# Performance work log

Hardware: AMD Instinct MI355X
Metric: run time of the kernel (lower is better)

The kernel has to match this reference:

```python
import jax, jax.numpy as jnp
import numpy as np

N_NODES = 50000
N_EDGES = 200000
D_FEAT = 512
D_HID = 1024


def setup_inputs() -> dict:
    key = jax.random.key(0)
    k_x, k_s, k_d, k_w1, k_w2 = jax.random.split(key, 5)
    x = jax.random.normal(k_x, (N_NODES, D_FEAT), dtype=jnp.float32)
    src = jax.random.randint(k_s, (N_EDGES,), 0, N_NODES, dtype=jnp.int64)
    dst = jax.random.randint(k_d, (N_EDGES,), 0, N_NODES, dtype=jnp.int64)
    # MLP params: Linear(2d -> hidden), ReLU, Linear(hidden -> 1)
    W1 = jax.random.normal(k_w1, (2 * D_FEAT, D_HID), dtype=jnp.float32) * (1.0 / np.sqrt(2 * D_FEAT))
    b1 = jnp.zeros((D_HID,), dtype=jnp.float32)
    W2 = jax.random.normal(k_w2, (D_HID, 1), dtype=jnp.float32) * (1.0 / np.sqrt(D_HID))
    b2 = jnp.zeros((1,), dtype=jnp.float32)
    return {"x": x, "src": src, "dst": dst, "W1": W1, "b1": b1, "W2": W2, "b2": b2}


def reference(x, src, dst, W1, b1, W2, b2):
    # Per-edge gather of src/dst node embeddings, concat along feature dim
    h = jnp.concatenate([x[src], x[dst]], axis=1)          # [E, 2d]
    h = jax.nn.relu(h @ W1 + b1)                            # [E, hidden]
    score = h @ W2 + b2                                     # [E, 1]
    return score
```

## Files before the change

### kernel.cpp

```cpp
#include <hip/hip_runtime.h>
#include <cstdint>
#include <cstddef>

typedef __attribute__((ext_vector_type(8))) short short8;
typedef __attribute__((ext_vector_type(4))) float f32x4;

#define D_FEAT 512
#define D_HID  1024
#define NCOL   2048
#define NCHUNK 32

__device__ __forceinline__ unsigned short f2bf(float f) {
    unsigned u = __builtin_bit_cast(unsigned, f);
    u += 0x7FFFu + ((u >> 16) & 1u);
    return (unsigned short)(u >> 16);
}

#define FENCE() asm volatile("" ::: "memory")
#define BAR()   do { FENCE(); __builtin_amdgcn_s_barrier(); FENCE(); } while (0)

__global__ __launch_bounds__(256) void cast_x_kernel(const float* __restrict__ x,
                                                     unsigned short* __restrict__ xb,
                                                     int n) {
    int i = (blockIdx.x * 256 + threadIdx.x) * 8;
    if (i >= n) return;
    const float4* xp = (const float4*)(x + i);
    float4 a = xp[0], b = xp[1];
    short8 o;
    o[0] = (short)f2bf(a.x); o[1] = (short)f2bf(a.y);
    o[2] = (short)f2bf(a.z); o[3] = (short)f2bf(a.w);
    o[4] = (short)f2bf(b.x); o[5] = (short)f2bf(b.y);
    o[6] = (short)f2bf(b.z); o[7] = (short)f2bf(b.w);
    *(short8*)(xb + i) = o;
}

__global__ __launch_bounds__(256) void transpose_w1_kernel(const float* __restrict__ W1,
                                                           unsigned short* __restrict__ w1t) {
    __shared__ float tile[32][33];
    const int half = blockIdx.z;
    const int kb = blockIdx.y * 32;
    const int nb = blockIdx.x * 32;
    const int tx = threadIdx.x, ty = threadIdx.y;
    #pragma unroll
    for (int i = 0; i < 32; i += 8)
        tile[ty + i][tx] = W1[(size_t)(half * 512 + kb + ty + i) * 1024 + nb + tx];
    __syncthreads();
    #pragma unroll
    for (int i = 0; i < 32; i += 8)
        w1t[(size_t)(half * 1024 + nb + ty + i) * 512 + kb + tx] = f2bf(tile[tx][ty + i]);
}

#define BM 256
#define BN 256
#define BK 64
#define GM 32
#define NB2 (NCOL / BN)

__global__ __launch_bounds__(512, 2) void gemm_uv_kernel(
    const unsigned short* __restrict__ xb,
    const unsigned short* __restrict__ w1t,
    const float* __restrict__ b1,
    unsigned char* __restrict__ qUV,
    float* __restrict__ scales,
    int M, int MB)
{
    __shared__ __align__(16) unsigned short smem[65536];

    const int bid = blockIdx.x;
    int g    = bid / (GM * NB2);
    int rem  = bid - g * (GM * NB2);
    int base = g * GM;
    int gm   = MB - base; if (gm > GM) gm = GM;
    int mb   = base + rem % gm;
    int nb   = rem / gm;
    const int m0 = mb * BM;
    const int n0 = nb * BN;

    const int tid  = threadIdx.x;
    const int wave = tid >> 6;
    const int lane = tid & 63;
    const int q    = lane >> 4;
    const int l15  = lane & 15;
    const int wr   = wave >> 2;
    const int wc   = wave & 3;

    const int ar    = lane >> 3;
    const int swcol = ((lane & 7) ^ ar) * 8;
    const int swz   = l15 & 7;

    const int slotA0 = wr * 16 + wc * 4;
    int bslot[4];
    bslot[0] = wc * 8 + wr * 2;     bslot[1] = bslot[0] + 1;
    bslot[2] = wc * 8 + 4 + wr * 2; bslot[3] = bslot[2] + 1;

    int rowA[4], rowB[4];
    #pragma unroll
    for (int j = 0; j < 4; ++j) {
        int m = m0 + (slotA0 + j) * 8 + ar;
        rowA[j] = (m < M) ? m : (M - 1);
        rowB[j] = n0 + bslot[j] * 8 + ar;
    }

    unsigned short* const sAbuf[2] = { smem,         smem + 16384 };
    unsigned short* const sBbuf[2] = { smem + 32768, smem + 49152 };

    auto stageA2 = [&](int t, int cb, int j0) {
        const int k0 = t * BK;
        #pragma unroll
        for (int j = 0; j < 2; ++j)
            __builtin_amdgcn_global_load_lds(
                (const __attribute__((address_space(1))) void*)(xb + ((size_t)rowA[j0 + j] << 9) + k0 + swcol),
                (__attribute__((address_space(3))) void*)(sAbuf[cb] + (slotA0 + j0 + j) * 512),
                16, 0, 0);
    };
    auto stageB2 = [&](int t, int cb, int j0) {
        const int k0 = t * BK;
        #pragma unroll
        for (int j = 0; j < 2; ++j)
            __builtin_amdgcn_global_load_lds(
                (const __attribute__((address_space(1))) void*)(w1t + ((size_t)rowB[j0 + j] << 9) + k0 + swcol),
                (__attribute__((address_space(3))) void*)(sBbuf[cb] + bslot[j0 + j] * 512),
                16, 0, 0);
    };
    auto readA = [&](int cb, int mt, int ks) -> short8 {
        int row = wr * 128 + mt * 16 + l15;
        return *(const short8*)(sAbuf[cb] + row * 64 + (((q | (ks << 2)) ^ swz) * 8));
    };
    auto readB = [&](int cb, int nt, int ks) -> short8 {
        int row = wc * 64 + nt * 16 + l15;
        return *(const short8*)(sBbuf[cb] + row * 64 + (((q | (ks << 2)) ^ swz) * 8));
    };

    float b1v[4];
    #pragma unroll
    for (int nt = 0; nt < 4; ++nt) {
        int n = n0 + wc * 64 + nt * 16 + l15;
        b1v[nt] = (n < D_HID) ? b1[n] : 0.f;
    }
    f32x4 acc[8][4];
    #pragma unroll
    for (int i = 0; i < 8; ++i)
        #pragma unroll
        for (int j = 0; j < 4; ++j)
            acc[i][j] = (f32x4){b1v[j], b1v[j], b1v[j], b1v[j]};

    stageA2(0, 0, 0);
    stageA2(0, 0, 2);
    stageB2(0, 0, 0);
    stageB2(0, 0, 2);
    stageA2(1, 1, 0);
    asm volatile("s_waitcnt vmcnt(4)" ::: "memory");
    BAR();

    short8 aR[4][2], bA[2][2], bB[2][2];

    #pragma unroll
    for (int t = 0; t < 8; ++t) {
        const int c = t & 1;

        #pragma unroll
        for (int mt = 0; mt < 4; ++mt)
            #pragma unroll
            for (int ks = 0; ks < 2; ++ks)
                aR[mt][ks] = readA(c, mt, ks);
        #pragma unroll
        for (int nt = 0; nt < 2; ++nt)
            #pragma unroll
            for (int ks = 0; ks < 2; ++ks)
                bA[nt][ks] = readB(c, nt, ks);
        if (t < 7) stageA2(t + 1, c ^ 1, 2);
        BAR();
        __builtin_amdgcn_s_setprio(1);
        #pragma unroll
        for (int ks = 0; ks < 2; ++ks)
            #pragma unroll
            for (int mt = 0; mt < 4; ++mt)
                #pragma unroll
                for (int nt = 0; nt < 2; ++nt)
                    acc[mt][nt] = __builtin_amdgcn_mfma_f32_16x16x32_bf16(aR[mt][ks], bA[nt][ks], acc[mt][nt], 0, 0, 0);
        __builtin_amdgcn_s_setprio(0);
        if (t < 7) { asm volatile("s_waitcnt vmcnt(4)" ::: "memory"); }
        else       { asm volatile("s_waitcnt vmcnt(0)" ::: "memory"); }
        BAR();

        #pragma unroll
        for (int nt = 0; nt < 2; ++nt)
            #pragma unroll
            for (int ks = 0; ks < 2; ++ks)
                bB[nt][ks] = readB(c, 2 + nt, ks);
        if (t < 7) stageB2(t + 1, c ^ 1, 0);
        BAR();
        __builtin_amdgcn_s_setprio(1);
        #pragma unroll
        for (int ks = 0; ks < 2; ++ks)
            #pragma unroll
            for (int mt = 0; mt < 4; ++mt)
                #pragma unroll
                for (int nt = 0; nt < 2; ++nt)
                    acc[mt][2 + nt] = __builtin_amdgcn_mfma_f32_16x16x32_bf16(aR[mt][ks], bB[nt][ks], acc[mt][2 + nt], 0, 0, 0);
        __builtin_amdgcn_s_setprio(0);
        BAR();

        #pragma unroll
        for (int mt = 0; mt < 4; ++mt)
            #pragma unroll
            for (int ks = 0; ks < 2; ++ks)
                aR[mt][ks] = readA(c, 4 + mt, ks);
        if (t < 7) stageB2(t + 1, c ^ 1, 2);
        BAR();
        __builtin_amdgcn_s_setprio(1);
        #pragma unroll
        for (int ks = 0; ks < 2; ++ks)
            #pragma unroll
            for (int mt = 0; mt < 4; ++mt)
                #pragma unroll
                for (int nt = 0; nt < 2; ++nt)
                    acc[4 + mt][nt] = __builtin_amdgcn_mfma_f32_16x16x32_bf16(aR[mt][ks], bA[nt][ks], acc[4 + mt][nt], 0, 0, 0);
        __builtin_amdgcn_s_setprio(0);
        BAR();

        if (t < 6) stageA2(t + 2, c, 0);
        BAR();
        __builtin_amdgcn_s_setprio(1);
        #pragma unroll
        for (int ks = 0; ks < 2; ++ks)
            #pragma unroll
            for (int mt = 0; mt < 4; ++mt)
                #pragma unroll
                for (int nt = 0; nt < 2; ++nt)
                    acc[4 + mt][2 + nt] = __builtin_amdgcn_mfma_f32_16x16x32_bf16(aR[mt][ks], bB[nt][ks], acc[4 + mt][2 + nt], 0, 0, 0);
        __builtin_amdgcn_s_setprio(0);
        if (t < 6)      { asm volatile("s_waitcnt vmcnt(4)" ::: "memory"); }
        else if (t == 6){ asm volatile("s_waitcnt vmcnt(2)" ::: "memory"); }
        BAR();
    }

    float msc[8], minv[8];
    #pragma unroll
    for (int mt = 0; mt < 8; ++mt) {
        float m_ = 1e-30f;
        #pragma unroll
        for (int nt = 0; nt < 4; ++nt)
            #pragma unroll
            for (int r = 0; r < 4; ++r)
                m_ = fmaxf(m_, fabsf(acc[mt][nt][r]));
        #pragma unroll
        for (int off = 1; off < 64; off <<= 1)
            m_ = fmaxf(m_, __shfl_xor(m_, off));
        msc[mt]  = m_ * (1.0f / 127.0f);
        minv[mt] = 127.0f * __builtin_amdgcn_rcpf(m_);
    }

    unsigned char* ep8 = (unsigned char*)smem + wave * 8192;
    const float MAGIC = 12583040.0f;
    #pragma unroll
    for (int mt = 0; mt < 8; ++mt)
        #pragma unroll
        for (int nt = 0; nt < 4; ++nt)
            #pragma unroll
            for (int r = 0; r < 4; ++r) {
                float f = fmaf(acc[mt][nt][r], minv[mt], MAGIC);
                ep8[(mt * 16 + q * 4 + r) * 64 + ((nt ^ q) * 16) + l15] =
                    (unsigned char)__builtin_bit_cast(unsigned, f);
            }
    const int chunk = (n0 + wc * 64) >> 6;
    #pragma unroll
    for (int h = 0; h < 2; ++h) {
        int srow = m0 + wr * 128 + h * 64 + q * 16 + l15;
        if (srow < M) scales[(size_t)srow * NCHUNK + chunk] = msc[h * 4 + q];
    }
    #pragma unroll
    for (int it = 0; it < 8; ++it) {
        int flat = it * 64 + lane;
        int r   = flat >> 2;
        int cI  = flat & 3;
        int m   = m0 + wr * 128 + r;
        if (m < M) {
            int4 v = *(const int4*)(ep8 + r * 64 + ((cI ^ ((r >> 2) & 3)) * 16));
            *(int4*)(qUV + (size_t)m * NCOL + n0 + wc * 64 + cI * 16) = v;
        }
    }
}

__global__ __launch_bounds__(256) void edge_score_kernel(
    const unsigned char* __restrict__ qUV,
    const float* __restrict__ scales,
    const int* __restrict__ src, const int* __restrict__ dst,
    const float* __restrict__ W2, const float* __restrict__ b2,
    float* __restrict__ out, int E)
{
    const int wave = threadIdx.x >> 6;
    const int lane = threadIdx.x & 63;
    const int gw = blockIdx.x * 4 + wave;
    const int e0 = gw * 2;
    const int e1 = e0 + 1;
    if (e0 >= E) return;
    const bool has1 = (e1 < E);

    const int s0 = src[e0];
    const int d0 = dst[e0];
    const int s1 = has1 ? src[e1] : s0;
    const int d1 = has1 ? dst[e1] : d0;

    uint4 qu0 = *(const uint4*)(qUV + (size_t)s0 * NCOL + lane * 16);
    uint4 qv0 = *(const uint4*)(qUV + (size_t)d0 * NCOL + D_HID + lane * 16);
    uint4 qu1 = *(const uint4*)(qUV + (size_t)s1 * NCOL + lane * 16);
    uint4 qv1 = *(const uint4*)(qUV + (size_t)d1 * NCOL + D_HID + lane * 16);
    const int ch = lane >> 2;
    float su0 = scales[(size_t)s0 * NCHUNK + ch];
    float sv0 = scales[(size_t)d0 * NCHUNK + 16 + ch];
    float su1 = scales[(size_t)s1 * NCHUNK + ch];
    float sv1 = scales[(size_t)d1 * NCHUNK + 16 + ch];
    float cc0 = -128.0f * (su0 + sv0);
    float cc1 = -128.0f * (su1 + sv1);

    const float4* wp = (const float4*)(W2 + lane * 16);
    float4 wa = wp[0], wb = wp[1], wc = wp[2], wd = wp[3];
    float w[16] = {wa.x, wa.y, wa.z, wa.w, wb.x, wb.y, wb.z, wb.w,
                   wc.x, wc.y, wc.z, wc.w, wd.x, wd.y, wd.z, wd.w};
    const float bias = b2[0];

    const unsigned* u0w = (const unsigned*)&qu0; const unsigned* v0w = (const unsigned*)&qv0;
    const unsigned* u1w = (const unsigned*)&qu1; const unsigned* v1w = (const unsigned*)&qv1;

    float acc0 = 0.f, acc1 = 0.f;
    #pragma unroll
    for (int dw = 0; dw < 4; ++dw) {
        #pragma unroll
        for (int b = 0; b < 4; ++b) {
            int k = dw * 4 + b;
            float ub0 = (float)((u0w[dw] >> (8 * b)) & 0xFFu);
            float vb0 = (float)((v0w[dw] >> (8 * b)) & 0xFFu);
            float h0 = fmaf(ub0, su0, fmaf(vb0, sv0, cc0));
            acc0 = fmaf(fmaxf(h0, 0.f), w[k], acc0);
            float ub1 = (float)((u1w[dw] >> (8 * b)) & 0xFFu);
            float vb1 = (float)((v1w[dw] >> (8 * b)) & 0xFFu);
            float h1 = fmaf(ub1, su1, fmaf(vb1, sv1, cc1));
            acc1 = fmaf(fmaxf(h1, 0.f), w[k], acc1);
        }
    }
    #pragma unroll
    for (int off = 1; off < 64; off <<= 1) {
        acc0 += __shfl_xor(acc0, off);
        acc1 += __shfl_xor(acc1, off);
    }
    if (lane == 0) out[e0] = acc0 + bias;
    if (lane == 1 && has1) out[e1] = acc1 + bias;
}

extern "C" void kernel_launch(void* const* d_in, const int* in_sizes, int n_in,
                              void* d_out, int out_size, void* d_ws, size_t ws_size,
                              hipStream_t stream) {
    const float* x   = (const float*)d_in[0];
    const int*   src = (const int*)d_in[1];
    const int*   dst = (const int*)d_in[2];
    const float* W1  = (const float*)d_in[3];
    const float* b1  = (const float*)d_in[4];
    const float* W2  = (const float*)d_in[5];
    const float* b2  = (const float*)d_in[6];
    float* out = (float*)d_out;

    const int M = in_sizes[0] / D_FEAT;
    const int E = in_sizes[1];

    char* ws = (char*)d_ws;
    unsigned char*  qUV    = (unsigned char*)ws;
    float*          scales = (float*)(ws + (size_t)M * NCOL);
    unsigned short* xb     = (unsigned short*)(ws + (size_t)M * NCOL + (size_t)M * NCHUNK * 4);
    unsigned short* w1t    = (unsigned short*)(ws + (size_t)M * NCOL + (size_t)M * NCHUNK * 4
                                                  + (size_t)M * D_FEAT * 2);

    const int nx = M * D_FEAT;
    cast_x_kernel<<<(nx / 8 + 255) / 256, 256, 0, stream>>>(x, xb, nx);
    transpose_w1_kernel<<<dim3(32, 16, 2), dim3(32, 8), 0, stream>>>(W1, w1t);
    const int MB = (M + BM - 1) / BM;
    gemm_uv_kernel<<<MB * NB2, 512, 0, stream>>>(xb, w1t, b1, qUV, scales, M, MB);
    edge_score_kernel<<<(E + 7) / 8, 256, 0, stream>>>(qUV, scales, src, dst, W2, b2, out, E);
}
```

Baseline: 363.1 us.

## Make GEMM persistent with epilogue/prefetch overlap and merge prep kernels

Merges the x cast and W1 transpose into a single prep launch. The GEMM becomes a persistent kernel with 256 blocks, each looping over M-tiles with a stride of 32. It issues the next tile's first stage loads before running the quantization epilogue of the current tile, and uses separate LDS regions for the epilogue so the two can overlap. This is meant to cut launch overhead and hide the epilogue and tail latency. In exchange it drops the grouped M-tile swizzle and the deeper two-ahead A prefetch inside the k-loop, which could hurt L2 reuse or load pipelining.

After: 477.5 us. 1.32x slower.

```diff
diff --git a/kernel.cpp b/kernel.cpp
--- a/kernel.cpp
+++ b/kernel.cpp
@@ -19,41 +19,44 @@
 #define FENCE() asm volatile("" ::: "memory")
 #define BAR()   do { FENCE(); __builtin_amdgcn_s_barrier(); FENCE(); } while (0)
 
-__global__ __launch_bounds__(256) void cast_x_kernel(const float* __restrict__ x,
-                                                     unsigned short* __restrict__ xb,
-                                                     int n) {
-    int i = (blockIdx.x * 256 + threadIdx.x) * 8;
-    if (i >= n) return;
-    const float4* xp = (const float4*)(x + i);
-    float4 a = xp[0], b = xp[1];
-    short8 o;
-    o[0] = (short)f2bf(a.x); o[1] = (short)f2bf(a.y);
-    o[2] = (short)f2bf(a.z); o[3] = (short)f2bf(a.w);
-    o[4] = (short)f2bf(b.x); o[5] = (short)f2bf(b.y);
-    o[6] = (short)f2bf(b.z); o[7] = (short)f2bf(b.w);
-    *(short8*)(xb + i) = o;
-}
-
-__global__ __launch_bounds__(256) void transpose_w1_kernel(const float* __restrict__ W1,
-                                                           unsigned short* __restrict__ w1t) {
-    __shared__ float tile[32][33];
-    const int half = blockIdx.z;
-    const int kb = blockIdx.y * 32;
-    const int nb = blockIdx.x * 32;
-    const int tx = threadIdx.x, ty = threadIdx.y;
-    #pragma unroll
-    for (int i = 0; i < 32; i += 8)
-        tile[ty + i][tx] = W1[(size_t)(half * 512 + kb + ty + i) * 1024 + nb + tx];
-    __syncthreads();
-    #pragma unroll
-    for (int i = 0; i < 32; i += 8)
-        w1t[(size_t)(half * 1024 + nb + ty + i) * 512 + kb + tx] = f2bf(tile[tx][ty + i]);
+#define NCAST 12500
+
+__global__ __launch_bounds__(256) void prep_kernel(const float* __restrict__ x,
+                                                   unsigned short* __restrict__ xb,
+                                                   const float* __restrict__ W1,
+                                                   unsigned short* __restrict__ w1t,
+                                                   int n) {
+    if ((int)blockIdx.x < NCAST) {
+        int i = (blockIdx.x * 256 + threadIdx.x) * 8;
+        if (i >= n) return;
+        const float4* xp = (const float4*)(x + i);
+        float4 a = xp[0], b = xp[1];
+        short8 o;
+        o[0] = (short)f2bf(a.x); o[1] = (short)f2bf(a.y);
+        o[2] = (short)f2bf(a.z); o[3] = (short)f2bf(a.w);
+        o[4] = (short)f2bf(b.x); o[5] = (short)f2bf(b.y);
+        o[6] = (short)f2bf(b.z); o[7] = (short)f2bf(b.w);
+        *(short8*)(xb + i) = o;
+    } else {
+        __shared__ float tile[32][33];
+        const int bid2 = blockIdx.x - NCAST;
+        const int half = bid2 >> 9;
+        const int kb   = ((bid2 >> 5) & 15) * 32;
+        const int nb   = (bid2 & 31) * 32;
+        const int tx = threadIdx.x & 31, ty = threadIdx.x >> 5;
+        #pragma unroll
+        for (int i = 0; i < 32; i += 8)
+            tile[ty + i][tx] = W1[(size_t)(half * 512 + kb + ty + i) * 1024 + nb + tx];
+        __syncthreads();
+        #pragma unroll
+        for (int i = 0; i < 32; i += 8)
+            w1t[(size_t)(half * 1024 + nb + ty + i) * 512 + kb + tx] = f2bf(tile[tx][ty + i]);
+    }
 }
 
 #define BM 256
 #define BN 256
 #define BK 64
-#define GM 32
 #define NB2 (NCOL / BN)
 
 __global__ __launch_bounds__(512, 2) void gemm_uv_kernel(
@@ -62,18 +65,13 @@
     const float* __restrict__ b1,
     unsigned char* __restrict__ qUV,
     float* __restrict__ scales,
-    int M, int MB)
+    int M, int MBT)
 {
     __shared__ __align__(16) unsigned short smem[65536];
 
-    const int bid = blockIdx.x;
-    int g    = bid / (GM * NB2);
-    int rem  = bid - g * (GM * NB2);
-    int base = g * GM;
-    int gm   = MB - base; if (gm > GM) gm = GM;
-    int mb   = base + rem % gm;
-    int nb   = rem / gm;
-    const int m0 = mb * BM;
+    const int b  = blockIdx.x;
+    const int nb = b & 7;
+    const int bq = b >> 3;
     const int n0 = nb * BN;
 
     const int tid  = threadIdx.x;
@@ -95,11 +93,8 @@
 
     int rowA[4], rowB[4];
     #pragma unroll
-    for (int j = 0; j < 4; ++j) {
-        int m = m0 + (slotA0 + j) * 8 + ar;
-        rowA[j] = (m < M) ? m : (M - 1);
+    for (int j = 0; j < 4; ++j)
         rowB[j] = n0 + bslot[j] * 8 + ar;
-    }
 
     unsigned short* const sAbuf[2] = { smem,         smem + 16384 };
     unsigned short* const sBbuf[2] = { smem + 32768, smem + 49152 };
@@ -144,140 +139,169 @@
         for (int j = 0; j < 4; ++j)
             acc[i][j] = (f32x4){b1v[j], b1v[j], b1v[j], b1v[j]};
 
-    stageA2(0, 0, 0);
-    stageA2(0, 0, 2);
-    stageB2(0, 0, 0);
-    stageB2(0, 0, 2);
-    stageA2(1, 1, 0);
-    asm volatile("s_waitcnt vmcnt(4)" ::: "memory");
+    const float MAGIC = 12583040.0f;
+    unsigned char* ep8 = (unsigned char*)smem +
+        ((wave < 4) ? (32768 + wave * 8192) : (98304 + (wave - 4) * 8192));
+    const int chunk = (n0 + wc * 64) >> 6;
+
+    int mb = bq;
+    #pragma unroll
+    for (int j = 0; j < 4; ++j) {
+        int m = mb * BM + (slotA0 + j) * 8 + ar;
+        rowA[j] = (m < M) ? m : (M - 1);
+    }
+    stageA2(0, 0, 0); stageA2(0, 0, 2); stageB2(0, 0, 0); stageB2(0, 0, 2);
+    asm volatile("s_waitcnt vmcnt(2)" ::: "memory");
     BAR();
 
-    short8 aR[4][2], bA[2][2], bB[2][2];
-
-    #pragma unroll
-    for (int t = 0; t < 8; ++t) {
-        const int c = t & 1;
-
-        #pragma unroll
-        for (int mt = 0; mt < 4; ++mt)
+    for (; mb < MBT; mb += 32) {
+        const int m0 = mb * BM;
+
+        short8 aR[4][2], bA[2][2], bB[2][2];
+        #pragma unroll
+        for (int t = 0; t < 8; ++t) {
+            const int c = t & 1;
+
+            #pragma unroll
+            for (int mt = 0; mt < 4; ++mt)
+                #pragma unroll
+                for (int ks = 0; ks < 2; ++ks)
+                    aR[mt][ks] = readA(c, mt, ks);
+            #pragma unroll
+            for (int nt = 0; nt < 2; ++nt)
+                #pragma unroll
+                for (int ks = 0; ks < 2; ++ks)
+                    bA[nt][ks] = readB(c, nt, ks);
+            if (t < 7) stageA2(t + 1, c ^ 1, 0);
+            BAR();
+            __builtin_amdgcn_s_setprio(1);
             #pragma unroll
             for (int ks = 0; ks < 2; ++ks)
-                aR[mt][ks] = readA(c, mt, ks);
-        #pragma unroll
-        for (int nt = 0; nt < 2; ++nt)
+                #pragma unroll
+                for (int mt = 0; mt < 4; ++mt)
+                    #pragma unroll
+                    for (int nt = 0; nt < 2; ++nt)
+                        acc[mt][nt] = __builtin_amdgcn_mfma_f32_16x16x32_bf16(aR[mt][ks], bA[nt][ks], acc[mt][nt], 0, 0, 0);
+            __builtin_amdgcn_s_setprio(0);
+            if (t < 7) { asm volatile("s_waitcnt vmcnt(2)" ::: "memory"); }
+            else       { asm volatile("s_waitcnt vmcnt(0)" ::: "memory"); }
+            BAR();
+
+            #pragma unroll
+            for (int nt = 0; nt < 2; ++nt)
+                #pragma unroll
+                for (int ks = 0; ks < 2; ++ks)
+                    bB[nt][ks] = readB(c, 2 + nt, ks);
+            if (t < 7) stageA2(t + 1, c ^ 1, 2);
+            BAR();
+            __builtin_amdgcn_s_setprio(1);
             #pragma unroll
             for (int ks = 0; ks < 2; ++ks)
-                bA[nt][ks] = readB(c, nt, ks);
-        if (t < 7) stageA2(t + 1, c ^ 1, 2);
+                #pragma unroll
+                for (int mt = 0; mt < 4; ++mt)
+                    #pragma unroll
+                    for (int nt = 0; nt < 2; ++nt)
+                        acc[mt][2 + nt] = __builtin_amdgcn_mfma_f32_16x16x32_bf16(aR[mt][ks], bB[nt][ks], acc[mt][2 + nt], 0, 0, 0);
+            __builtin_amdgcn_s_setprio(0);
+            BAR();
+
+            #pragma unroll
+            for (int mt = 0; mt < 4; ++mt)
+                #pragma unroll
+                for (int ks = 0; ks < 2; ++ks)
+                    aR[mt][ks] = readA(c, 4 + mt, ks);
+            if (t < 7) stageB2(t + 1, c ^ 1, 0);
+            BAR();
+            __builtin_amdgcn_s_setprio(1);
+            #pragma unroll
+            for (int ks = 0; ks < 2; ++ks)
+                #pragma unroll
+                for (int mt = 0; mt < 4; ++mt)
+                    #pragma unroll
+                    for (int nt = 0; nt < 2; ++nt)
+                        acc[4 + mt][nt] = __builtin_amdgcn_mfma_f32_16x16x32_bf16(aR[mt][ks], bA[nt][ks], acc[4 + mt][nt], 0, 0, 0);
+            __builtin_amdgcn_s_setprio(0);
+            BAR();
+
+            if (t < 7) stageB2(t + 1, c ^ 1, 2);
+            BAR();
+            __builtin_amdgcn_s_setprio(1);
+            #pragma unroll
+            for (int ks = 0; ks < 2; ++ks)
+                #pragma unroll
+                for (int mt = 0; mt < 4; ++mt)
+                    #pragma unroll
+                    for (int nt = 0; nt < 2; ++nt)
+                        acc[4 + mt][2 + nt] = __builtin_amdgcn_mfma_f32_16x16x32_bf16(aR[mt][ks], bB[nt][ks], acc[4 + mt][2 + nt], 0, 0, 0);
+            __builtin_amdgcn_s_setprio(0);
+            if (t < 7) { asm volatile("s_waitcnt vmcnt(2)" ::: "memory"); }
+            BAR();
+        }
+
+        const int mbn = mb + 32;
+        const bool hn = (mbn < MBT);
+        if (hn) {
+            #pragma unroll
+            for (int j = 0; j < 4; ++j) {
+                int m = mbn * BM + (slotA0 + j) * 8 + ar;
+                rowA[j] = (m < M) ? m : (M - 1);
+            }
+            stageA2(0, 0, 0); stageA2(0, 0, 2); stageB2(0, 0, 0); stageB2(0, 0, 2);
+        }
+
+        float msc[8], minv[8];
+        #pragma unroll
+        for (int mt = 0; mt < 8; ++mt) {
+            float m_ = 1e-30f;
+            #pragma unroll
+            for (int nt = 0; nt < 4; ++nt)
+                #pragma unroll
+                for (int r = 0; r < 4; ++r)
+                    m_ = fmaxf(m_, fabsf(acc[mt][nt][r]));
+            #pragma unroll
+            for (int off = 1; off < 64; off <<= 1)
+                m_ = fmaxf(m_, __shfl_xor(m_, off));
+            msc[mt]  = m_ * (1.0f / 127.0f);
+            minv[mt] = 127.0f * __builtin_amdgcn_rcpf(m_);
+        }
+        #pragma unroll
+        for (int mt = 0; mt < 8; ++mt)
+            #pragma unroll
+            for (int nt = 0; nt < 4; ++nt)
+                #pragma unroll
+                for (int r = 0; r < 4; ++r) {
+                    float f = fmaf(acc[mt][nt][r], minv[mt], MAGIC);
+                    ep8[(mt * 16 + q * 4 + r) * 64 + ((nt ^ q) * 16) + l15] =
+                        (unsigned char)__builtin_bit_cast(unsigned, f);
+                }
+        #pragma unroll
+        for (int h = 0; h < 2; ++h) {
+            int srow = m0 + wr * 128 + h * 64 + q * 16 + l15;
+            if (srow < M) scales[(size_t)srow * NCHUNK + chunk] = msc[h * 4 + q];
+        }
+        #pragma unroll
+        for (int it = 0; it < 8; ++it) {
+            int flat = it * 64 + lane;
+            int r   = flat >> 2;
+            int cI  = flat & 3;
+            int m   = m0 + wr * 128 + r;
+            if (m < M) {
+                int4 v = *(const int4*)(ep8 + r * 64 + ((cI ^ ((r >> 2) & 3)) * 16));
+                *(int4*)(qUV + (size_t)m * NCOL + n0 + wc * 64 + cI * 16) = v;
+            }
+        }
+
+        if (hn) {
+            asm volatile("s_waitcnt vmcnt(10)" ::: "memory");
+        }
         BAR();
-        __builtin_amdgcn_s_setprio(1);
-        #pragma unroll
-        for (int ks = 0; ks < 2; ++ks)
-            #pragma unroll
-            for (int mt = 0; mt < 4; ++mt)
-                #pragma unroll
-                for (int nt = 0; nt < 2; ++nt)
-                    acc[mt][nt] = __builtin_amdgcn_mfma_f32_16x16x32_bf16(aR[mt][ks], bA[nt][ks], acc[mt][nt], 0, 0, 0);
-        __builtin_amdgcn_s_setprio(0);
-        if (t < 7) { asm volatile("s_waitcnt vmcnt(4)" ::: "memory"); }
-        else       { asm volatile("s_waitcnt vmcnt(0)" ::: "memory"); }
-        BAR();
-
-        #pragma unroll
-        for (int nt = 0; nt < 2; ++nt)
-            #pragma unroll
-            for (int ks = 0; ks < 2; ++ks)
-                bB[nt][ks] = readB(c, 2 + nt, ks);
-        if (t < 7) stageB2(t + 1, c ^ 1, 0);
-        BAR();
-        __builtin_amdgcn_s_setprio(1);
-        #pragma unroll
-        for (int ks = 0; ks < 2; ++ks)
-            #pragma unroll
-            for (int mt = 0; mt < 4; ++mt)
-                #pragma unroll
-                for (int nt = 0; nt < 2; ++nt)
-                    acc[mt][2 + nt] = __builtin_amdgcn_mfma_f32_16x16x32_bf16(aR[mt][ks], bB[nt][ks], acc[mt][2 + nt], 0, 0, 0);
-        __builtin_amdgcn_s_setprio(0);
-        BAR();
-
-        #pragma unroll
-        for (int mt = 0; mt < 4; ++mt)
-            #pragma unroll
-            for (int ks = 0; ks < 2; ++ks)
-                aR[mt][ks] = readA(c, 4 + mt, ks);
-        if (t < 7) stageB2(t + 1, c ^ 1, 2);
-        BAR();
-        __builtin_amdgcn_s_setprio(1);
-        #pragma unroll
-        for (int ks = 0; ks < 2; ++ks)
-            #pragma unroll
-            for (int mt = 0; mt < 4; ++mt)
-                #pragma unroll
-                for (int nt = 0; nt < 2; ++nt)
-                    acc[4 + mt][nt] = __builtin_amdgcn_mfma_f32_16x16x32_bf16(aR[mt][ks], bA[nt][ks], acc[4 + mt][nt], 0, 0, 0);
-        __builtin_amdgcn_s_setprio(0);
-        BAR();
-
-        if (t < 6) stageA2(t + 2, c, 0);
-        BAR();
-        __builtin_amdgcn_s_setprio(1);
-        #pragma unroll
-        for (int ks = 0; ks < 2; ++ks)
-            #pragma unroll
-            for (int mt = 0; mt < 4; ++mt)
-                #pragma unroll
-                for (int nt = 0; nt < 2; ++nt)
-                    acc[4 + mt][2 + nt] = __builtin_amdgcn_mfma_f32_16x16x32_bf16(aR[mt][ks], bB[nt][ks], acc[4 + mt][2 + nt], 0, 0, 0);
-        __builtin_amdgcn_s_setprio(0);
-        if (t < 6)      { asm volatile("s_waitcnt vmcnt(4)" ::: "memory"); }
-        else if (t == 6){ asm volatile("s_waitcnt vmcnt(2)" ::: "memory"); }
-        BAR();
-    }
-
-    float msc[8], minv[8];
-    #pragma unroll
-    for (int mt = 0; mt < 8; ++mt) {
-        float m_ = 1e-30f;
-        #pragma unroll
-        for (int nt = 0; nt < 4; ++nt)
-            #pragma unroll
-            for (int r = 0; r < 4; ++r)
-                m_ = fmaxf(m_, fabsf(acc[mt][nt][r]));
-        #pragma unroll
-        for (int off = 1; off < 64; off <<= 1)
-            m_ = fmaxf(m_, __shfl_xor(m_, off));
-        msc[mt]  = m_ * (1.0f / 127.0f);
-        minv[mt] = 127.0f * __builtin_amdgcn_rcpf(m_);
-    }
-
-    unsigned char* ep8 = (unsigned char*)smem + wave * 8192;
-    const float MAGIC = 12583040.0f;
-    #pragma unroll
-    for (int mt = 0; mt < 8; ++mt)
-        #pragma unroll
-        for (int nt = 0; nt < 4; ++nt)
-            #pragma unroll
-            for (int r = 0; r < 4; ++r) {
-                float f = fmaf(acc[mt][nt][r], minv[mt], MAGIC);
-                ep8[(mt * 16 + q * 4 + r) * 64 + ((nt ^ q) * 16) + l15] =
-                    (unsigned char)__builtin_bit_cast(unsigned, f);
-            }
-    const int chunk = (n0 + wc * 64) >> 6;
-    #pragma unroll
-    for (int h = 0; h < 2; ++h) {
-        int srow = m0 + wr * 128 + h * 64 + q * 16 + l15;
-        if (srow < M) scales[(size_t)srow * NCHUNK + chunk] = msc[h * 4 + q];
-    }
-    #pragma unroll
-    for (int it = 0; it < 8; ++it) {
-        int flat = it * 64 + lane;
-        int r   = flat >> 2;
-        int cI  = flat & 3;
-        int m   = m0 + wr * 128 + r;
-        if (m < M) {
-            int4 v = *(const int4*)(ep8 + r * 64 + ((cI ^ ((r >> 2) & 3)) * 16));
-            *(int4*)(qUV + (size_t)m * NCOL + n0 + wc * 64 + cI * 16) = v;
+
+        if (hn) {
+            #pragma unroll
+            for (int i = 0; i < 8; ++i)
+                #pragma unroll
+                for (int j = 0; j < 4; ++j)
+                    acc[i][j] = (f32x4){b1v[j], b1v[j], b1v[j], b1v[j]};
         }
     }
 }
@@ -371,9 +395,8 @@
                                                   + (size_t)M * D_FEAT * 2);
 
     const int nx = M * D_FEAT;
-    cast_x_kernel<<<(nx / 8 + 255) / 256, 256, 0, stream>>>(x, xb, nx);
-    transpose_w1_kernel<<<dim3(32, 16, 2), dim3(32, 8), 0, stream>>>(W1, w1t);
-    const int MB = (M + BM - 1) / BM;
-    gemm_uv_kernel<<<MB * NB2, 512, 0, stream>>>(xb, w1t, b1, qUV, scales, M, MB);
+    prep_kernel<<<NCAST + 1024, 256, 0, stream>>>(x, xb, W1, w1t, nx);
+    const int MBT = (M + BM - 1) / BM;
+    gemm_uv_kernel<<<256, 512, 0, stream>>>(xb, w1t, b1, qUV, scales, M, MBT);
     edge_score_kernel<<<(E + 7) / 8, 256, 0, stream>>>(qUV, scales, src, dst, W2, b2, out, E);
 }
```
